# Optimization experiments

Measured on AMD Instinct MI355X. Metric: run time of the kernel, lower is better.

The kernel has to match this reference:

```python
import jax, jax.numpy as jnp
import numpy as np
from functools import partial

V, D, L, H, S, B, FF = 32000, 1024, 4, 16, 1024, 2, 4096
DH = D // H
PREFIX = 256
NSEG = 4
LN_EPS = 1e-5
NEG = -1e9


def _ln(x, g, b):
    m = jnp.mean(x, axis=-1, keepdims=True)
    v = jnp.mean(jnp.square(x - m), axis=-1, keepdims=True)
    return (x - m) * jax.lax.rsqrt(v + LN_EPS) * g + b


def setup_inputs() -> dict:
    key = jax.random.key(0)
    ks = jax.random.split(key, 12)
    wstd = 0.02
    inp = {}
    inp['input_ids'] = jax.random.randint(ks[0], (B, S), 0, V)
    inp['segment_ids'] = jnp.sort(jax.random.randint(ks[1], (B, S), 0, NSEG), axis=-1)
    # prefix tokens (bidirectional region): first PREFIX positions
    inp['attention_mask'] = jnp.broadcast_to(jnp.arange(S) < PREFIX, (B, S))
    inp['embedding'] = jax.random.normal(ks[2], (V, D), jnp.float32) / np.sqrt(D)
    inp['in_proj_w'] = jax.random.normal(ks[3], (L, 3 * D, D), jnp.float32) * wstd
    inp['in_proj_b'] = jnp.zeros((L, 3 * D), jnp.float32)
    inp['out_proj_w'] = jax.random.normal(ks[4], (L, D, D), jnp.float32) * wstd
    inp['out_proj_b'] = jnp.zeros((L, D), jnp.float32)
    inp['ln1_g'] = jnp.ones((L, D), jnp.float32)
    inp['ln1_b'] = jnp.zeros((L, D), jnp.float32)
    inp['ln2_g'] = jnp.ones((L, D), jnp.float32)
    inp['ln2_b'] = jnp.zeros((L, D), jnp.float32)
    inp['lin1_w'] = jax.random.normal(ks[5], (L, FF, D), jnp.float32) * wstd
    inp['lin1_b'] = jnp.zeros((L, FF), jnp.float32)
    inp['lin2_w'] = jax.random.normal(ks[6], (L, D, FF), jnp.float32) * wstd
    inp['lin2_b'] = jnp.zeros((L, D), jnp.float32)
    inp['normf_g'] = jnp.ones((D,), jnp.float32)
    inp['normf_b'] = jnp.zeros((D,), jnp.float32)
    inp['head_w'] = jax.random.normal(ks[7], (V, D), jnp.float32) / np.sqrt(D)
    inp['head_b'] = jnp.zeros((V,), jnp.float32)
    return inp


def reference(input_ids, segment_ids, attention_mask, embedding,
              in_proj_w, in_proj_b, out_proj_w, out_proj_b,
              ln1_g, ln1_b, ln2_g, ln2_b,
              lin1_w, lin1_b, lin2_w, lin2_b,
              normf_g, normf_b, head_w, head_b):
    b, s = input_ids.shape
    # combined prefix + causal + segment mask: True = allowed to attend
    causal = jnp.tril(jnp.ones((s, s), bool))                                  # (S,S)
    seg = segment_ids[:, :, None] == segment_ids[:, None, :]                   # (B,S,S)
    pref = attention_mask[:, :, None] & attention_mask[:, None, :]             # (B,S,S)
    allowed = (pref | causal[None]) & seg                                      # (B,S,S)

    x = embedding[input_ids]                                                   # (B,S,D)
    inv_sqrt_dh = 1.0 / np.sqrt(DH)

    def layer(x, p):
        wqkv, bqkv, wo, bo, g1, b1, g2, b2, w1, bb1, w2, bb2 = p
        # pre-norm self-attention (norm_first=True, dropout=0 / eval)
        h = _ln(x, g1, b1)
        qkv = h @ wqkv.T + bqkv                                                # (B,S,3D)
        q, k, v = jnp.split(qkv, 3, axis=-1)
        q = q.reshape(b, s, H, DH)
        k = k.reshape(b, s, H, DH)
        v = v.reshape(b, s, H, DH)
        scores = jnp.einsum('bqhd,bkhd->bhqk', q, k) * inv_sqrt_dh             # (B,H,S,S)
        scores = jnp.where(allowed[:, None], scores, NEG)
        a = jax.nn.softmax(scores, axis=-1)
        o = jnp.einsum('bhqk,bkhd->bqhd', a, v).reshape(b, s, D)
        x = x + o @ wo.T + bo
        # pre-norm FFN (exact-erf gelu per torch default)
        h2 = _ln(x, g2, b2)
        ff = jax.nn.gelu(h2 @ w1.T + bb1, approximate=False) @ w2.T + bb2
        return x + ff, None

    params = (in_proj_w, in_proj_b, out_proj_w, out_proj_b,
              ln1_g, ln1_b, ln2_g, ln2_b, lin1_w, lin1_b, lin2_w, lin2_b)
    x, _ = jax.lax.scan(layer, x, params)
    x = _ln(x, normf_g, normf_b)
    logits = x @ head_w.T + head_b                                             # (B,S,V)
    return logits
```

## Files before the change

### kernel.cpp

```cpp
#include <hip/hip_runtime.h>
#include <math.h>

#define S_ 1024
#define D_ 1024
#define H_ 16
#define DH_ 64
#define B_ 2
#define FF_ 4096
#define L_ 4
#define V_ 32000
#define PREFIX_ 256

using u16 = unsigned short;
typedef __attribute__((ext_vector_type(4))) u16 u16x4;
typedef __attribute__((ext_vector_type(8))) __bf16 bf16x8;
typedef __attribute__((ext_vector_type(4))) float f32x4;
typedef __attribute__((ext_vector_type(4))) float fx4;

__device__ __forceinline__ float b2f(u16 x) {
    return __uint_as_float(((unsigned)x) << 16);
}
__device__ __forceinline__ u16 f2bf(float f) {
    unsigned u = __float_as_uint(f);
    return (u16)((u + 0x7FFF + ((u >> 16) & 1)) >> 16);
}

__device__ __forceinline__ void async_lds16(const u16* g, u16* l) {
    __builtin_amdgcn_global_load_lds(
        (const __attribute__((address_space(1))) unsigned int*)g,
        (__attribute__((address_space(3))) unsigned int*)l,
        16, 0, 0);
}

template<int EPI>
__global__ __launch_bounds__(512, 2)
void gemm256(const u16* __restrict__ A, const u16* __restrict__ Bw,
             void* __restrict__ Cout, const float* __restrict__ bias,
             int K, int lda, int ldb, int ldc)
{
    extern __shared__ u16 lds[];
    const int tid = threadIdx.x;
    const int lane = tid & 63;
    const int wv = tid >> 6;
    const int wm = wv >> 2;
    const int wn = wv & 3;
    const int fr = lane & 15;
    const int fq = lane >> 4;

    const int nx = gridDim.x;
    int id = blockIdx.y * nx + blockIdx.x;
    const int nwg = nx * gridDim.y;
    if ((nwg & 7) == 0) { const int cpx = nwg >> 3; id = (id & 7) * cpx + (id >> 3); }
    const int m0 = (id / nx) * 256;
    const int n0 = (id % nx) * 256;

    const int r_in = lane >> 3;
    const int c_sw = ((lane & 7) ^ r_in) * 8;
    const u16* sA0 = A  + (size_t)(m0 + wv * 16 +     r_in) * lda + c_sw;
    const u16* sA1 = A  + (size_t)(m0 + wv * 16 + 8 + r_in) * lda + c_sw;
    const u16* sB0 = Bw + (size_t)(n0 + wv * 16 +     r_in) * ldb + c_sw;
    const u16* sB1 = Bw + (size_t)(n0 + wv * 16 + 8 + r_in) * ldb + c_sw;

    auto stageA = [&](int b, int h, int k0) {
        u16* d = lds + b * 16384 + h * 8192 + wv * 1024;
        async_lds16(sA0 + (size_t)h * 128 * lda + k0, d);
        async_lds16(sA1 + (size_t)h * 128 * lda + k0, d + 512);
    };
    auto stageB = [&](int b, int h, int k0) {
        u16* d = lds + 32768 + b * 16384 + h * 8192 + wv * 1024;
        async_lds16(sB0 + (size_t)h * 128 * ldb + k0, d);
        async_lds16(sB1 + (size_t)h * 128 * ldb + k0, d + 512);
    };
    auto readA = [&](int b, int h, int m, int ks) -> bf16x8 {
        const int r = wm * 64 + m * 16 + fr;
        const int col = (ks * 32 + fq * 8) ^ ((fr & 7) << 3);
        return *(const bf16x8*)&lds[b * 16384 + h * 8192 + r * 64 + col];
    };
    auto readB = [&](int b, int h, int n, int ks) -> bf16x8 {
        const int r = wn * 32 + n * 16 + fr;
        const int col = (ks * 32 + fq * 8) ^ ((fr & 7) << 3);
        return *(const bf16x8*)&lds[32768 + b * 16384 + h * 8192 + r * 64 + col];
    };

    f32x4 acc[2][2][4][2] = {};
    bf16x8 a[4][2], b0[2][2], b1[2][2];

#define VMW(n) asm volatile("s_waitcnt vmcnt(" #n ")" ::: "memory")
#define BAR() do { __builtin_amdgcn_sched_barrier(0); __builtin_amdgcn_s_barrier(); \
                   __builtin_amdgcn_sched_barrier(0); } while (0)
#define MFMA16(h, j, bb) do { \
    __builtin_amdgcn_s_setprio(1); \
    _Pragma("unroll") for (int m = 0; m < 4; ++m) \
    _Pragma("unroll") for (int n = 0; n < 2; ++n) \
    _Pragma("unroll") for (int ks = 0; ks < 2; ++ks) \
        acc[h][j][m][n] = __builtin_amdgcn_mfma_f32_16x16x32_bf16(a[m][ks], bb[n][ks], acc[h][j][m][n], 0, 0, 0); \
    __builtin_amdgcn_s_setprio(0); } while (0)

    const int NT = K >> 6;
    stageA(0, 0, 0); stageB(0, 0, 0); stageB(0, 1, 0); stageA(0, 1, 0);

    for (int t = 0; t < NT - 1; ++t) {
        const int cur = t & 1, nxt = cur ^ 1, k1 = (t + 1) << 6;
        VMW(4); BAR();
        #pragma unroll
        for (int m = 0; m < 4; ++m) { a[m][0] = readA(cur, 0, m, 0); a[m][1] = readA(cur, 0, m, 1); }
        #pragma unroll
        for (int n = 0; n < 2; ++n) { b0[n][0] = readB(cur, 0, n, 0); b0[n][1] = readB(cur, 0, n, 1); }
        stageA(nxt, 0, k1);
        MFMA16(0, 0, b0);
        VMW(4); BAR();
        #pragma unroll
        for (int n = 0; n < 2; ++n) { b1[n][0] = readB(cur, 1, n, 0); b1[n][1] = readB(cur, 1, n, 1); }
        stageB(nxt, 0, k1);
        MFMA16(0, 1, b1);
        VMW(4); BAR();
        #pragma unroll
        for (int m = 0; m < 4; ++m) { a[m][0] = readA(cur, 1, m, 0); a[m][1] = readA(cur, 1, m, 1); }
        stageB(nxt, 1, k1);
        MFMA16(1, 0, b0);
        VMW(4); BAR();
        stageA(nxt, 1, k1);
        MFMA16(1, 1, b1);
    }
    {
        const int cur = (NT - 1) & 1;
        VMW(4); BAR();
        #pragma unroll
        for (int m = 0; m < 4; ++m) { a[m][0] = readA(cur, 0, m, 0); a[m][1] = readA(cur, 0, m, 1); }
        #pragma unroll
        for (int n = 0; n < 2; ++n) { b0[n][0] = readB(cur, 0, n, 0); b0[n][1] = readB(cur, 0, n, 1); }
        MFMA16(0, 0, b0);
        VMW(2); BAR();
        #pragma unroll
        for (int n = 0; n < 2; ++n) { b1[n][0] = readB(cur, 1, n, 0); b1[n][1] = readB(cur, 1, n, 1); }
        MFMA16(0, 1, b1);
        VMW(0); BAR();
        #pragma unroll
        for (int m = 0; m < 4; ++m) { a[m][0] = readA(cur, 1, m, 0); a[m][1] = readA(cur, 1, m, 1); }
        MFMA16(1, 0, b0);
        MFMA16(1, 1, b1);
    }
#undef VMW
#undef BAR
#undef MFMA16

    #pragma unroll
    for (int h = 0; h < 2; ++h)
    #pragma unroll
    for (int j = 0; j < 2; ++j)
    #pragma unroll
    for (int m = 0; m < 4; ++m)
    #pragma unroll
    for (int n = 0; n < 2; ++n) {
        const int gr0 = m0 + h * 128 + wm * 64 + m * 16 + fq * 4;
        const int gc  = n0 + j * 128 + wn * 32 + n * 16 + fr;
        #pragma unroll
        for (int r = 0; r < 4; ++r) {
            const float v = acc[h][j][m][n][r];
            if (EPI == 0) {
                ((float*)Cout)[(size_t)(gr0 + r) * ldc + gc] = v + bias[gc];
            } else if (EPI == 5) {
                const float tt = v + bias[gc];
                const float g = 0.5f * tt * (1.0f + erff(tt * 0.70710678118654752f));
                ((u16*)Cout)[(size_t)(gr0 + r) * ldc + gc] = f2bf(g);
            }
        }
    }
}

template<int BM, int BN, int NWM, int NWN, int WM, int WN, int EPI>
__global__ __launch_bounds__(256)
void gemm_bt(const u16* __restrict__ A, const u16* __restrict__ Bw,
             void* __restrict__ Cout,
             const float* __restrict__ bias,
             const float* __restrict__ resid,
             const int* __restrict__ seg,
             int K, int lda, int ldb, int ldc,
             long sA, long sB, long sC)
{
    static_assert(NWM * NWN == 4, "4 waves");
    static_assert(BM == NWM * WM * 16 && BN == NWN * WN * 16, "tile");
    __shared__ __align__(16) u16 ldsA[BM * 32];
    __shared__ __align__(16) u16 ldsB[BN * 32];

    const int tid = threadIdx.x;
    const int z = blockIdx.z;

    const int nx = gridDim.x;
    int id = blockIdx.y * nx + blockIdx.x;
    const int nwg = nx * gridDim.y;
    if ((nwg & 7) == 0) {
        const int cpx = nwg >> 3;
        id = (id & 7) * cpx + (id >> 3);
    }
    const int m0 = (id / nx) * BM;
    const int n0 = (id % nx) * BN;

    const u16* Ab = A + (long)z * sA;
    const u16* Bb = Bw + (long)z * sB;

    const int lane = tid & 63;
    const int wv = tid >> 6;
    const int wm = wv / NWN;
    const int wn = wv % NWN;
    const int fr = lane & 15;
    const int fq = lane >> 4;

    f32x4 acc[WM][WN] = {};

    for (int k0 = 0; k0 < K; k0 += 32) {
        #pragma unroll
        for (int r = 0; r < BM / 64; ++r) {
            int c = tid + r * 256;
            int row = c >> 2, col = (c & 3) << 3;
            async_lds16(Ab + (long)(m0 + row) * lda + k0 + col, &ldsA[c * 8]);
        }
        #pragma unroll
        for (int r = 0; r < BN / 64; ++r) {
            int c = tid + r * 256;
            int row = c >> 2, col = (c & 3) << 3;
            async_lds16(Bb + (long)(n0 + row) * ldb + k0 + col, &ldsB[c * 8]);
        }
        __syncthreads();

        bf16x8 af[WM], bfr[WN];
        #pragma unroll
        for (int m = 0; m < WM; ++m)
            af[m] = *(const bf16x8*)&ldsA[(wm * WM * 16 + m * 16 + fr) * 32 + fq * 8];
        #pragma unroll
        for (int n = 0; n < WN; ++n)
            bfr[n] = *(const bf16x8*)&ldsB[(wn * WN * 16 + n * 16 + fr) * 32 + fq * 8];
        #pragma unroll
        for (int m = 0; m < WM; ++m)
            #pragma unroll
            for (int n = 0; n < WN; ++n)
                acc[m][n] = __builtin_amdgcn_mfma_f32_16x16x32_bf16(af[m], bfr[n], acc[m][n], 0, 0, 0);
        __syncthreads();
    }

    #pragma unroll
    for (int m = 0; m < WM; ++m) {
        const int gr0 = m0 + wm * WM * 16 + m * 16 + fq * 4;
        #pragma unroll
        for (int n = 0; n < WN; ++n) {
            const int gc = n0 + wn * WN * 16 + n * 16 + fr;
            #pragma unroll
            for (int r = 0; r < 4; ++r) {
                const int gr = gr0 + r;
                float v = acc[m][n][r];
                if (EPI == 1) {
                    ((u16*)Cout)[(long)z * sC + (long)gr * ldc + gc] = f2bf(v + bias[gc]);
                } else if (EPI == 2) {
                    const int b = z >> 4;
                    const int sq = seg[b * S_ + gr], sk = seg[b * S_ + gc];
                    const bool allowed = (sq == sk) &&
                        ((gr >= gc) || (gr < PREFIX_ && gc < PREFIX_));
                    ((u16*)Cout)[(long)z * sC + (long)gr * ldc + gc] = f2bf(allowed ? v : -1e9f);
                } else if (EPI == 3) {
                    const int b = z >> 4, hh = z & (H_ - 1);
                    ((u16*)Cout)[((long)(b * S_ + gr)) * D_ + hh * DH_ + gc] = f2bf(v);
                } else if (EPI == 4) {
                    const long idx = (long)gr * ldc + gc;
                    ((float*)Cout)[idx] = v + bias[gc] + resid[idx];
                }
            }
        }
    }
}

__global__ __launch_bounds__(256)
void ln_bf16_kernel(const float* __restrict__ x, const float* __restrict__ g,
                    const float* __restrict__ b, u16* __restrict__ out)
{
    const int row = blockIdx.x;
    const int t = threadIdx.x;
    fx4 xv = ((const fx4*)(x + (long)row * D_))[t];
    float s = xv[0] + xv[1] + xv[2] + xv[3];
    #pragma unroll
    for (int o = 32; o; o >>= 1) s += __shfl_down(s, o, 64);
    __shared__ float red[8];
    const int lane = t & 63, wv = t >> 6;
    if (lane == 0) red[wv] = s;
    __syncthreads();
    const float mean = (red[0] + red[1] + red[2] + red[3]) * (1.0f / D_);
    float d0 = xv[0] - mean, d1 = xv[1] - mean, d2 = xv[2] - mean, d3 = xv[3] - mean;
    float s2 = d0 * d0 + d1 * d1 + d2 * d2 + d3 * d3;
    #pragma unroll
    for (int o = 32; o; o >>= 1) s2 += __shfl_down(s2, o, 64);
    if (lane == 0) red[4 + wv] = s2;
    __syncthreads();
    const float var = (red[4] + red[5] + red[6] + red[7]) * (1.0f / D_);
    const float rstd = rsqrtf(var + 1e-5f);
    #pragma unroll
    for (int j = 0; j < 4; ++j) {
        const int c = t * 4 + j;
        out[(long)row * D_ + c] = f2bf((xv[j] - mean) * rstd * g[c] + b[c]);
    }
}

__global__ __launch_bounds__(256)
void softmax_kernel(u16* __restrict__ p)
{
    const long row = blockIdx.x;
    const int t = threadIdx.x;
    u16x4 raw = ((u16x4*)(p + row * S_))[t];
    float v0 = b2f(raw[0]), v1 = b2f(raw[1]), v2 = b2f(raw[2]), v3 = b2f(raw[3]);
    float mx = fmaxf(fmaxf(v0, v1), fmaxf(v2, v3));
    #pragma unroll
    for (int o = 32; o; o >>= 1) mx = fmaxf(mx, __shfl_down(mx, o, 64));
    __shared__ float red[8];
    const int lane = t & 63, wv = t >> 6;
    if (lane == 0) red[wv] = mx;
    __syncthreads();
    mx = fmaxf(fmaxf(red[0], red[1]), fmaxf(red[2], red[3]));
    v0 = expf(v0 - mx); v1 = expf(v1 - mx); v2 = expf(v2 - mx); v3 = expf(v3 - mx);
    float s = v0 + v1 + v2 + v3;
    #pragma unroll
    for (int o = 32; o; o >>= 1) s += __shfl_down(s, o, 64);
    if (lane == 0) red[4 + wv] = s;
    __syncthreads();
    const float inv = 1.0f / (red[4] + red[5] + red[6] + red[7]);
    u16x4 w;
    w[0] = f2bf(v0 * inv); w[1] = f2bf(v1 * inv);
    w[2] = f2bf(v2 * inv); w[3] = f2bf(v3 * inv);
    ((u16x4*)(p + row * S_))[t] = w;
}

__global__ __launch_bounds__(256)
void qkv_reorder_kernel(const u16* __restrict__ qkv, u16* __restrict__ q,
                        u16* __restrict__ k, u16* __restrict__ vT)
{
    const int p = blockIdx.x;
    const int b = p >> 10;
    const int s = p & (S_ - 1);
    const int t = threadIdx.x;
    const long base = (long)p * 3 * D_;
    #pragma unroll
    for (int j = 0; j < 4; ++j) {
        const int idx = t * 4 + j;
        const int hh = idx >> 6, d = idx & 63;
        u16 qv = qkv[base + idx];
        u16 kv = qkv[base + D_ + idx];
        u16 vv = qkv[base + 2 * D_ + idx];
        const long zh = (long)(b * H_ + hh);
        q[(zh * S_ + s) * DH_ + d] = f2bf(b2f(qv) * 0.125f);
        k[(zh * S_ + s) * DH_ + d] = kv;
        vT[(zh * DH_ + d) * S_ + s] = vv;
    }
}

__global__ __launch_bounds__(256)
void embed_kernel(const int* __restrict__ ids, const float* __restrict__ emb,
                  float* __restrict__ x)
{
    const int p = blockIdx.x;
    const int id = ids[p];
    ((fx4*)(x + (long)p * D_))[threadIdx.x] = ((const fx4*)(emb + (long)id * D_))[threadIdx.x];
}

__global__ __launch_bounds__(256)
void f32_to_bf16_kernel(const float* __restrict__ in, u16* __restrict__ out)
{
    const long i = ((long)blockIdx.x * 256 + threadIdx.x) * 4;
    fx4 v = *(const fx4*)(in + i);
    u16x4 o;
    o[0] = f2bf(v[0]); o[1] = f2bf(v[1]); o[2] = f2bf(v[2]); o[3] = f2bf(v[3]);
    *(u16x4*)(out + i) = o;
}

extern "C" void kernel_launch(void* const* d_in, const int* in_sizes, int n_in,
                              void* d_out, int out_size, void* d_ws, size_t ws_size,
                              hipStream_t stream)
{
    const int*   input_ids   = (const int*)d_in[0];
    const int*   segment_ids = (const int*)d_in[1];
    const float* embedding   = (const float*)d_in[3];
    const float* in_proj_w   = (const float*)d_in[4];
    const float* in_proj_b   = (const float*)d_in[5];
    const float* out_proj_w  = (const float*)d_in[6];
    const float* out_proj_b  = (const float*)d_in[7];
    const float* ln1_g       = (const float*)d_in[8];
    const float* ln1_b       = (const float*)d_in[9];
    const float* ln2_g       = (const float*)d_in[10];
    const float* ln2_b       = (const float*)d_in[11];
    const float* lin1_w      = (const float*)d_in[12];
    const float* lin1_b      = (const float*)d_in[13];
    const float* lin2_w      = (const float*)d_in[14];
    const float* lin2_b      = (const float*)d_in[15];
    const float* normf_g     = (const float*)d_in[16];
    const float* normf_b     = (const float*)d_in[17];
    const float* head_w      = (const float*)d_in[18];
    const float* head_b      = (const float*)d_in[19];
    float* out = (float*)d_out;

    (void)hipFuncSetAttribute((const void*)&gemm256<0>,
        hipFuncAttributeMaxDynamicSharedMemorySize, 131072);
    (void)hipFuncSetAttribute((const void*)&gemm256<5>,
        hipFuncAttributeMaxDynamicSharedMemorySize, 131072);

    char* wp = (char*)d_ws;
    auto alloc = [&](size_t n) { char* p = wp; wp += (n + 255) & ~(size_t)255; return p; };
    u16* wqkv = (u16*)alloc((size_t)L_ * 3 * D_ * D_ * 2);
    u16* wo   = (u16*)alloc((size_t)L_ * D_ * D_ * 2);
    u16* w1   = (u16*)alloc((size_t)L_ * FF_ * D_ * 2);
    u16* w2   = (u16*)alloc((size_t)L_ * D_ * FF_ * 2);
    u16* wh   = (u16*)alloc((size_t)V_ * D_ * 2);
    float* x  = (float*)alloc((size_t)B_ * S_ * D_ * 4);
    u16* h    = (u16*)alloc((size_t)B_ * S_ * D_ * 2);
    u16* qkv  = (u16*)alloc((size_t)B_ * S_ * 3 * D_ * 2);
    u16* q    = (u16*)alloc((size_t)B_ * H_ * S_ * DH_ * 2);
    u16* k    = (u16*)alloc((size_t)B_ * H_ * S_ * DH_ * 2);
    u16* vT   = (u16*)alloc((size_t)B_ * H_ * S_ * DH_ * 2);
    u16* sc   = (u16*)alloc((size_t)B_ * H_ * S_ * S_ * 2);
    u16* o    = (u16*)alloc((size_t)B_ * S_ * D_ * 2);
    u16* ff   = (u16*)alloc((size_t)B_ * S_ * FF_ * 2);

    f32_to_bf16_kernel<<<L_ * 3 * D_ * D_ / 1024, 256, 0, stream>>>(in_proj_w, wqkv);
    f32_to_bf16_kernel<<<L_ * D_ * D_ / 1024, 256, 0, stream>>>(out_proj_w, wo);
    f32_to_bf16_kernel<<<L_ * FF_ * D_ / 1024, 256, 0, stream>>>(lin1_w, w1);
    f32_to_bf16_kernel<<<L_ * D_ * FF_ / 1024, 256, 0, stream>>>(lin2_w, w2);
    f32_to_bf16_kernel<<<V_ * D_ / 1024, 256, 0, stream>>>(head_w, wh);

    embed_kernel<<<B_ * S_, 256, 0, stream>>>(input_ids, embedding, x);

    for (int l = 0; l < L_; ++l) {
        ln_bf16_kernel<<<B_ * S_, 256, 0, stream>>>(x, ln1_g + l * D_, ln1_b + l * D_, h);
        gemm_bt<128, 128, 2, 2, 4, 4, 1><<<dim3(3 * D_ / 128, B_ * S_ / 128, 1), 256, 0, stream>>>(
            h, wqkv + (long)l * 3 * D_ * D_, qkv, in_proj_b + l * 3 * D_, nullptr, nullptr,
            D_, D_, D_, 3 * D_, 0, 0, 0);
        qkv_reorder_kernel<<<B_ * S_, 256, 0, stream>>>(qkv, q, k, vT);
        gemm_bt<128, 128, 2, 2, 4, 4, 2><<<dim3(S_ / 128, S_ / 128, B_ * H_), 256, 0, stream>>>(
            q, k, sc, nullptr, nullptr, segment_ids,
            DH_, DH_, DH_, S_, (long)S_ * DH_, (long)S_ * DH_, (long)S_ * S_);
        softmax_kernel<<<B_ * H_ * S_, 256, 0, stream>>>(sc);
        gemm_bt<64, 64, 2, 2, 2, 2, 3><<<dim3(1, S_ / 64, B_ * H_), 256, 0, stream>>>(
            sc, vT, o, nullptr, nullptr, nullptr,
            S_, S_, S_, 0, (long)S_ * S_, (long)DH_ * S_, 0);
        gemm_bt<64, 128, 2, 2, 2, 4, 4><<<dim3(D_ / 128, B_ * S_ / 64, 1), 256, 0, stream>>>(
            o, wo + (long)l * D_ * D_, x, out_proj_b + l * D_, x, nullptr,
            D_, D_, D_, D_, 0, 0, 0);
        ln_bf16_kernel<<<B_ * S_, 256, 0, stream>>>(x, ln2_g + l * D_, ln2_b + l * D_, h);
        gemm256<5><<<dim3(FF_ / 256, B_ * S_ / 256), 512, 131072, stream>>>(
            h, w1 + (long)l * FF_ * D_, ff, lin1_b + l * FF_, D_, D_, D_, FF_);
        gemm_bt<64, 128, 2, 2, 2, 4, 4><<<dim3(D_ / 128, B_ * S_ / 64, 1), 256, 0, stream>>>(
            ff, w2 + (long)l * D_ * FF_, x, lin2_b + l * D_, x, nullptr,
            FF_, FF_, FF_, D_, 0, 0, 0);
    }

    ln_bf16_kernel<<<B_ * S_, 256, 0, stream>>>(x, normf_g, normf_b, h);
    gemm256<0><<<dim3(V_ / 256, B_ * S_ / 256), 512, 131072, stream>>>(
        h, wh, out, head_b, D_, D_, D_, V_);
}
```

Measured before the change: 1.400 ms.

## Replace score/softmax/PV attention pipeline with fused flash attention kernel

Adds a flash-attention kernel that computes QK^T, the segment/causal/prefix mask, an online softmax and the PV product in registers and LDS, with double-buffered K/V tiles and causal tile skipping. This removes the materialized B*H*S*S bf16 score matrix and its round trips through the separate masked-GEMM, softmax and PV kernels. It also switches the FFN1 GEMM from the 256-tile kernel to the 128-tile gemm_bt with a GELU epilogue, and changes the tile rasterization in both GEMM kernels to column-major order. The new attention kernel uses small per-wave tiles and adds shuffle-reduction overhead, and the FFN1 kernel change may be slower than the larger-tile kernel.

```diff
diff --git a/kernel.cpp b/kernel.cpp
--- a/kernel.cpp
+++ b/kernel.cpp
@@ -47,12 +47,12 @@
     const int fr = lane & 15;
     const int fq = lane >> 4;
 
-    const int nx = gridDim.x;
+    const int nx = gridDim.x, ny = gridDim.y;
     int id = blockIdx.y * nx + blockIdx.x;
-    const int nwg = nx * gridDim.y;
+    const int nwg = nx * ny;
     if ((nwg & 7) == 0) { const int cpx = nwg >> 3; id = (id & 7) * cpx + (id >> 3); }
-    const int m0 = (id / nx) * 256;
-    const int n0 = (id % nx) * 256;
+    const int m0 = (id % ny) * 256;
+    const int n0 = (id / ny) * 256;
 
     const int r_in = lane >> 3;
     const int c_sw = ((lane & 7) ^ r_in) * 8;
@@ -168,15 +168,192 @@
     }
 }
 
+__global__ __launch_bounds__(256)
+void flash_attn_kernel(const u16* __restrict__ q, const u16* __restrict__ kk,
+                       const u16* __restrict__ vT, const int* __restrict__ seg,
+                       u16* __restrict__ o)
+{
+    __shared__ __align__(16) u16 k_lds[2][64 * 64];
+    __shared__ __align__(16) u16 v_lds[2][64 * 64];
+    __shared__ __align__(16) u16 p_lds[4][32 * 64];
+    __shared__ int seg_lds[S_];
+
+    const int tid = threadIdx.x;
+    const int lane = tid & 63, wv = tid >> 6;
+    const int fr = lane & 15, fq = lane >> 4;
+    const int z = blockIdx.z, b = z >> 4, hh = z & 15;
+    const int q0 = blockIdx.x * 128;
+
+    const u16* qz = q  + (size_t)z * S_ * DH_;
+    const u16* kz = kk + (size_t)z * S_ * DH_;
+    const u16* vz = vT + (size_t)z * DH_ * S_;
+
+    {
+        const int* sb = seg + b * S_;
+        #pragma unroll
+        for (int j = 0; j < 4; ++j) seg_lds[tid + j * 256] = sb[tid + j * 256];
+    }
+    bf16x8 qf[2][2];
+    #pragma unroll
+    for (int m = 0; m < 2; ++m)
+        #pragma unroll
+        for (int c = 0; c < 2; ++c)
+            qf[m][c] = *(const bf16x8*)(qz + (size_t)(q0 + wv * 32 + m * 16 + fr) * DH_ + c * 32 + fq * 8);
+
+    const int u0 = (wv * 2) * 64 + lane, u1 = (wv * 2 + 1) * 64 + lane;
+    const int r0 = u0 >> 3, c0 = ((u0 & 7) ^ (r0 & 7)) << 3;
+    const int r1 = u1 >> 3, c1 = ((u1 & 7) ^ (r1 & 7)) << 3;
+
+    auto stage = [&](int buf, int kt) {
+        async_lds16(kz + (size_t)(kt * 64 + r0) * DH_ + c0, &k_lds[buf][u0 * 8]);
+        async_lds16(kz + (size_t)(kt * 64 + r1) * DH_ + c1, &k_lds[buf][u1 * 8]);
+        async_lds16(vz + (size_t)r0 * S_ + kt * 64 + c0, &v_lds[buf][u0 * 8]);
+        async_lds16(vz + (size_t)r1 * S_ + kt * 64 + c1, &v_lds[buf][u1 * 8]);
+    };
+
+    f32x4 oacc[2][4] = {};
+    float mrun[2][4], lrun[2][4];
+    int qi[2][4], sq[2][4]; bool qp[2][4];
+
+    stage(0, 0);
+    __syncthreads();
+
+    #pragma unroll
+    for (int m = 0; m < 2; ++m)
+        #pragma unroll
+        for (int rr = 0; rr < 4; ++rr) {
+            const int qrow = q0 + wv * 32 + m * 16 + fq * 4 + rr;
+            qi[m][rr] = qrow; sq[m][rr] = seg_lds[qrow]; qp[m][rr] = qrow < PREFIX_;
+            mrun[m][rr] = -1e30f; lrun[m][rr] = 0.f;
+        }
+
+    const int nkt0 = (q0 >> 6) + 2;
+    const int nkt = nkt0 > 4 ? nkt0 : 4;
+
+    for (int kt = 0; kt < nkt; ++kt) {
+        const int buf = kt & 1;
+        if (kt + 1 < nkt) stage(buf ^ 1, kt + 1);
+
+        bf16x8 kf_[4][2];
+        #pragma unroll
+        for (int n = 0; n < 4; ++n)
+            #pragma unroll
+            for (int c = 0; c < 2; ++c) {
+                const int r = n * 16 + fr;
+                kf_[n][c] = *(const bf16x8*)&k_lds[buf][r * 64 + ((c * 32 + fq * 8) ^ ((r & 7) << 3))];
+            }
+        f32x4 sacc[2][4] = {};
+        #pragma unroll
+        for (int m = 0; m < 2; ++m)
+            #pragma unroll
+            for (int n = 0; n < 4; ++n)
+                #pragma unroll
+                for (int c = 0; c < 2; ++c)
+                    sacc[m][n] = __builtin_amdgcn_mfma_f32_16x16x32_bf16(qf[m][c], kf_[n][c], sacc[m][n], 0, 0, 0);
+
+        int ki[4], sk[4]; bool kp[4];
+        #pragma unroll
+        for (int n = 0; n < 4; ++n) {
+            ki[n] = kt * 64 + n * 16 + fr;
+            sk[n] = seg_lds[ki[n]];
+            kp[n] = ki[n] < PREFIX_;
+        }
+        #pragma unroll
+        for (int m = 0; m < 2; ++m)
+            #pragma unroll
+            for (int n = 0; n < 4; ++n)
+                #pragma unroll
+                for (int rr = 0; rr < 4; ++rr) {
+                    const bool ok = (sq[m][rr] == sk[n]) &&
+                        ((qi[m][rr] >= ki[n]) || (qp[m][rr] && kp[n]));
+                    if (!ok) sacc[m][n][rr] = -3e38f;
+                }
+
+        #pragma unroll
+        for (int m = 0; m < 2; ++m)
+            #pragma unroll
+            for (int rr = 0; rr < 4; ++rr) {
+                float v = fmaxf(fmaxf(sacc[m][0][rr], sacc[m][1][rr]),
+                                fmaxf(sacc[m][2][rr], sacc[m][3][rr]));
+                v = fmaxf(v, __shfl_xor(v, 1, 64));
+                v = fmaxf(v, __shfl_xor(v, 2, 64));
+                v = fmaxf(v, __shfl_xor(v, 4, 64));
+                v = fmaxf(v, __shfl_xor(v, 8, 64));
+                const float mnew = fmaxf(mrun[m][rr], v);
+                const float alpha = __expf(mrun[m][rr] - mnew);
+                mrun[m][rr] = mnew;
+                float rs = 0.f;
+                #pragma unroll
+                for (int n = 0; n < 4; ++n) {
+                    const float p = __expf(sacc[m][n][rr] - mnew);
+                    sacc[m][n][rr] = p;
+                    rs += p;
+                }
+                rs += __shfl_xor(rs, 1, 64);
+                rs += __shfl_xor(rs, 2, 64);
+                rs += __shfl_xor(rs, 4, 64);
+                rs += __shfl_xor(rs, 8, 64);
+                lrun[m][rr] = lrun[m][rr] * alpha + rs;
+                #pragma unroll
+                for (int n = 0; n < 4; ++n) oacc[m][n][rr] *= alpha;
+            }
+
+        #pragma unroll
+        for (int m = 0; m < 2; ++m)
+            #pragma unroll
+            for (int n = 0; n < 4; ++n)
+                #pragma unroll
+                for (int rr = 0; rr < 4; ++rr) {
+                    const int row = m * 16 + fq * 4 + rr;
+                    const int col = (n * 16 + fr) ^ ((row & 7) << 3);
+                    p_lds[wv][row * 64 + col] = f2bf(sacc[m][n][rr]);
+                }
+        bf16x8 pf[2][2], vf[4][2];
+        #pragma unroll
+        for (int m = 0; m < 2; ++m)
+            #pragma unroll
+            for (int c = 0; c < 2; ++c) {
+                const int r = m * 16 + fr;
+                pf[m][c] = *(const bf16x8*)&p_lds[wv][r * 64 + ((c * 32 + fq * 8) ^ ((r & 7) << 3))];
+            }
+        #pragma unroll
+        for (int n = 0; n < 4; ++n)
+            #pragma unroll
+            for (int c = 0; c < 2; ++c) {
+                const int r = n * 16 + fr;
+                vf[n][c] = *(const bf16x8*)&v_lds[buf][r * 64 + ((c * 32 + fq * 8) ^ ((r & 7) << 3))];
+            }
+        #pragma unroll
+        for (int m = 0; m < 2; ++m)
+            #pragma unroll
+            for (int n = 0; n < 4; ++n)
+                #pragma unroll
+                for (int c = 0; c < 2; ++c)
+                    oacc[m][n] = __builtin_amdgcn_mfma_f32_16x16x32_bf16(pf[m][c], vf[n][c], oacc[m][n], 0, 0, 0);
+
+        __syncthreads();
+    }
+
+    #pragma unroll
+    for (int m = 0; m < 2; ++m)
+        #pragma unroll
+        for (int rr = 0; rr < 4; ++rr) {
+            const float inv = 1.0f / lrun[m][rr];
+            const int srow = q0 + wv * 32 + m * 16 + fq * 4 + rr;
+            #pragma unroll
+            for (int n = 0; n < 4; ++n)
+                o[((size_t)(b * S_ + srow)) * D_ + hh * 64 + n * 16 + fr] =
+                    f2bf(oacc[m][n][rr] * inv);
+        }
+}
+
 template<int BM, int BN, int NWM, int NWN, int WM, int WN, int EPI>
 __global__ __launch_bounds__(256)
 void gemm_bt(const u16* __restrict__ A, const u16* __restrict__ Bw,
              void* __restrict__ Cout,
              const float* __restrict__ bias,
              const float* __restrict__ resid,
-             const int* __restrict__ seg,
-             int K, int lda, int ldb, int ldc,
-             long sA, long sB, long sC)
+             int K, int lda, int ldb, int ldc)
 {
     static_assert(NWM * NWN == 4, "4 waves");
     static_assert(BM == NWM * WM * 16 && BN == NWN * WN * 16, "tile");
@@ -184,20 +361,15 @@
     __shared__ __align__(16) u16 ldsB[BN * 32];
 
     const int tid = threadIdx.x;
-    const int z = blockIdx.z;
-
-    const int nx = gridDim.x;
+    const int nx = gridDim.x, ny = gridDim.y;
     int id = blockIdx.y * nx + blockIdx.x;
-    const int nwg = nx * gridDim.y;
+    const int nwg = nx * ny;
     if ((nwg & 7) == 0) {
         const int cpx = nwg >> 3;
         id = (id & 7) * cpx + (id >> 3);
     }
-    const int m0 = (id / nx) * BM;
-    const int n0 = (id % nx) * BN;
-
-    const u16* Ab = A + (long)z * sA;
-    const u16* Bb = Bw + (long)z * sB;
+    const int m0 = (id % ny) * BM;
+    const int n0 = (id / ny) * BN;
 
     const int lane = tid & 63;
     const int wv = tid >> 6;
@@ -213,13 +385,13 @@
         for (int r = 0; r < BM / 64; ++r) {
             int c = tid + r * 256;
             int row = c >> 2, col = (c & 3) << 3;
-            async_lds16(Ab + (long)(m0 + row) * lda + k0 + col, &ldsA[c * 8]);
+            async_lds16(A + (long)(m0 + row) * lda + k0 + col, &ldsA[c * 8]);
         }
         #pragma unroll
         for (int r = 0; r < BN / 64; ++r) {
             int c = tid + r * 256;
             int row = c >> 2, col = (c & 3) << 3;
-            async_lds16(Bb + (long)(n0 + row) * ldb + k0 + col, &ldsB[c * 8]);
+            async_lds16(Bw + (long)(n0 + row) * ldb + k0 + col, &ldsB[c * 8]);
         }
         __syncthreads();
 
@@ -249,19 +421,14 @@
                 const int gr = gr0 + r;
                 float v = acc[m][n][r];
                 if (EPI == 1) {
-                    ((u16*)Cout)[(long)z * sC + (long)gr * ldc + gc] = f2bf(v + bias[gc]);
-                } else if (EPI == 2) {
-                    const int b = z >> 4;
-                    const int sq = seg[b * S_ + gr], sk = seg[b * S_ + gc];
-                    const bool allowed = (sq == sk) &&
-                        ((gr >= gc) || (gr < PREFIX_ && gc < PREFIX_));
-                    ((u16*)Cout)[(long)z * sC + (long)gr * ldc + gc] = f2bf(allowed ? v : -1e9f);
-                } else if (EPI == 3) {
-                    const int b = z >> 4, hh = z & (H_ - 1);
-                    ((u16*)Cout)[((long)(b * S_ + gr)) * D_ + hh * DH_ + gc] = f2bf(v);
+                    ((u16*)Cout)[(long)gr * ldc + gc] = f2bf(v + bias[gc]);
                 } else if (EPI == 4) {
                     const long idx = (long)gr * ldc + gc;
                     ((float*)Cout)[idx] = v + bias[gc] + resid[idx];
+                } else if (EPI == 5) {
+                    float t = v + bias[gc];
+                    float g = 0.5f * t * (1.0f + erff(t * 0.70710678118654752f));
+                    ((u16*)Cout)[(long)gr * ldc + gc] = f2bf(g);
                 }
             }
         }
@@ -296,34 +463,6 @@
         const int c = t * 4 + j;
         out[(long)row * D_ + c] = f2bf((xv[j] - mean) * rstd * g[c] + b[c]);
     }
-}
-
-__global__ __launch_bounds__(256)
-void softmax_kernel(u16* __restrict__ p)
-{
-    const long row = blockIdx.x;
-    const int t = threadIdx.x;
-    u16x4 raw = ((u16x4*)(p + row * S_))[t];
-    float v0 = b2f(raw[0]), v1 = b2f(raw[1]), v2 = b2f(raw[2]), v3 = b2f(raw[3]);
-    float mx = fmaxf(fmaxf(v0, v1), fmaxf(v2, v3));
-    #pragma unroll
-    for (int o = 32; o; o >>= 1) mx = fmaxf(mx, __shfl_down(mx, o, 64));
-    __shared__ float red[8];
-    const int lane = t & 63, wv = t >> 6;
-    if (lane == 0) red[wv] = mx;
-    __syncthreads();
-    mx = fmaxf(fmaxf(red[0], red[1]), fmaxf(red[2], red[3]));
-    v0 = expf(v0 - mx); v1 = expf(v1 - mx); v2 = expf(v2 - mx); v3 = expf(v3 - mx);
-    float s = v0 + v1 + v2 + v3;
-    #pragma unroll
-    for (int o = 32; o; o >>= 1) s += __shfl_down(s, o, 64);
-    if (lane == 0) red[4 + wv] = s;
-    __syncthreads();
-    const float inv = 1.0f / (red[4] + red[5] + red[6] + red[7]);
-    u16x4 w;
-    w[0] = f2bf(v0 * inv); w[1] = f2bf(v1 * inv);
-    w[2] = f2bf(v2 * inv); w[3] = f2bf(v3 * inv);
-    ((u16x4*)(p + row * S_))[t] = w;
 }
 
 __global__ __launch_bounds__(256)
@@ -395,8 +534,6 @@
 
     (void)hipFuncSetAttribute((const void*)&gemm256<0>,
         hipFuncAttributeMaxDynamicSharedMemorySize, 131072);
-    (void)hipFuncSetAttribute((const void*)&gemm256<5>,
-        hipFuncAttributeMaxDynamicSharedMemorySize, 131072);
 
     char* wp = (char*)d_ws;
     auto alloc = [&](size_t n) { char* p = wp; wp += (n + 255) & ~(size_t)255; return p; };
@@ -411,7 +548,6 @@
     u16* q    = (u16*)alloc((size_t)B_ * H_ * S_ * DH_ * 2);
     u16* k    = (u16*)alloc((size_t)B_ * H_ * S_ * DH_ * 2);
     u16* vT   = (u16*)alloc((size_t)B_ * H_ * S_ * DH_ * 2);
-    u16* sc   = (u16*)alloc((size_t)B_ * H_ * S_ * S_ * 2);
     u16* o    = (u16*)alloc((size_t)B_ * S_ * D_ * 2);
     u16* ff   = (u16*)alloc((size_t)B_ * S_ * FF_ * 2);
 
@@ -426,25 +562,21 @@
     for (int l = 0; l < L_; ++l) {
         ln_bf16_kernel<<<B_ * S_, 256, 0, stream>>>(x, ln1_g + l * D_, ln1_b + l * D_, h);
         gemm_bt<128, 128, 2, 2, 4, 4, 1><<<dim3(3 * D_ / 128, B_ * S_ / 128, 1), 256, 0, stream>>>(
-            h, wqkv + (long)l * 3 * D_ * D_, qkv, in_proj_b + l * 3 * D_, nullptr, nullptr,
-            D_, D_, D_, 3 * D_, 0, 0, 0);
+            h, wqkv + (long)l * 3 * D_ * D_, qkv, in_proj_b + l * 3 * D_, nullptr,
+            D_, D_, D_, 3 * D_);
         qkv_reorder_kernel<<<B_ * S_, 256, 0, stream>>>(qkv, q, k, vT);
-        gemm_bt<128, 128, 2, 2, 4, 4, 2><<<dim3(S_ / 128, S_ / 128, B_ * H_), 256, 0, stream>>>(
-            q, k, sc, nullptr, nullptr, segment_ids,
-            DH_, DH_, DH_, S_, (long)S_ * DH_, (long)S_ * DH_, (long)S_ * S_);
-        softmax_kernel<<<B_ * H_ * S_, 256, 0, stream>>>(sc);
-        gemm_bt<64, 64, 2, 2, 2, 2, 3><<<dim3(1, S_ / 64, B_ * H_), 256, 0, stream>>>(
-            sc, vT, o, nullptr, nullptr, nullptr,
-            S_, S_, S_, 0, (long)S_ * S_, (long)DH_ * S_, 0);
+        flash_attn_kernel<<<dim3(S_ / 128, 1, B_ * H_), 256, 0, stream>>>(
+            q, k, vT, segment_ids, o);
         gemm_bt<64, 128, 2, 2, 2, 4, 4><<<dim3(D_ / 128, B_ * S_ / 64, 1), 256, 0, stream>>>(
-            o, wo + (long)l * D_ * D_, x, out_proj_b + l * D_, x, nullptr,
-            D_, D_, D_, D_, 0, 0, 0);
+            o, wo + (long)l * D_ * D_, x, out_proj_b + l * D_, x,
+            D_, D_, D_, D_);
         ln_bf16_kernel<<<B_ * S_, 256, 0, stream>>>(x, ln2_g + l * D_, ln2_b + l * D_, h);
-        gemm256<5><<<dim3(FF_ / 256, B_ * S_ / 256), 512, 131072, stream>>>(
-            h, w1 + (long)l * FF_ * D_, ff, lin1_b + l * FF_, D_, D_, D_, FF_);
+        gemm_bt<128, 128, 2, 2, 4, 4, 5><<<dim3(FF_ / 128, B_ * S_ / 128, 1), 256, 0, stream>>>(
+            h, w1 + (long)l * FF_ * D_, ff, lin1_b + l * FF_, nullptr,
+            D_, D_, D_, FF_);
         gemm_bt<64, 128, 2, 2, 2, 4, 4><<<dim3(D_ / 128, B_ * S_ / 64, 1), 256, 0, stream>>>(
-            ff, w2 + (long)l * D_ * FF_, x, lin2_b + l * D_, x, nullptr,
-            FF_, FF_, FF_, D_, 0, 0, 0);
+            ff, w2 + (long)l * D_ * FF_, x, lin2_b + l * D_, x,
+            FF_, FF_, FF_, D_);
     }
 
     ln_bf16_kernel<<<B_ * S_, 256, 0, stream>>>(x, normf_g, normf_b, h);
```

Result: no change. 1.390 ms (-0.7%).
